# Kernel optimization log

Measured on AMD Instinct MI355X. Metric: run time of the kernel, lower is better.

The kernel has to match this reference:

```python
import jax, jax.numpy as jnp
import numpy as np

B, N, C, H = 4, 2048, 384, 8
HD = C // H  # 48; divisible by 6 so RoPE3D splits into three even-sized chunks
ROPE_BASE = 100.0  # RoPE3D(100)


def _rope1d(x, p):
    # x: [B,H,N,d], p: [B,N] integer positions
    d = x.shape[-1]
    inv = 1.0 / (ROPE_BASE ** (jnp.arange(0, d, 2, dtype=jnp.float32) / d))  # [d/2]
    ang = p[:, None, :, None].astype(jnp.float32) * inv                      # [B,1,N,d/2]
    ang = jnp.concatenate([ang, ang], axis=-1)                               # [B,1,N,d]
    cos, sin = jnp.cos(ang), jnp.sin(ang)
    x1, x2 = jnp.split(x, 2, axis=-1)
    return x * cos + jnp.concatenate([-x2, x1], axis=-1) * sin


def _rope3d(x, pos):
    # x: [B,H,N,D], pos: [B,N,3]; rotate each D/3 chunk by one spatial axis
    parts = jnp.split(x, 3, axis=-1)
    return jnp.concatenate([_rope1d(parts[i], pos[..., i]) for i in range(3)], axis=-1)


def setup_inputs() -> dict:
    key = jax.random.key(0)
    ks = jax.random.split(key, 9)
    T = B * N
    s = 1.0 / np.sqrt(C).astype(np.float32)
    offs = jnp.arange(1, B + 1, dtype=jnp.int32) * N  # equal-length segments
    return {
        "query": jax.random.normal(ks[0], (T, C), jnp.float32),
        "key": jax.random.normal(ks[1], (T, C), jnp.float32),
        "value": jax.random.normal(ks[2], (T, C), jnp.float32),
        "Wq": jax.random.normal(ks[3], (C, C), jnp.float32) * s,
        "bq": jnp.zeros((C,), jnp.float32),
        "Wk": jax.random.normal(ks[4], (C, C), jnp.float32) * s,
        "bk": jnp.zeros((C,), jnp.float32),
        "Wv": jax.random.normal(ks[5], (C, C), jnp.float32) * s,
        "bv": jnp.zeros((C,), jnp.float32),
        "Wo": jax.random.normal(ks[6], (C, C), jnp.float32) * s,
        "bo": jnp.zeros((C,), jnp.float32),
        "qpos": jax.random.randint(ks[7], (T, 3), 0, 100),
        "kpos": jax.random.randint(ks[8], (T, 3), 0, 100),
        "src_point_offset": offs,
        "tgt_point_offset": offs,
    }


def reference(query, key, value, Wq, bq, Wk, bk, Wv, bv, Wo, bo,
              qpos, kpos, src_point_offset, tgt_point_offset):
    # Equal-length segments (offsets = [N,2N,...]) => the per-item python loop
    # in forward_pcd_to_pcd is exactly one batched attention over [B,N,C].
    qb = query.reshape(B, N, C)
    kb = key.reshape(B, N, C)
    vb = value.reshape(B, N, C)
    q = (qb @ Wq.T + bq).reshape(B, N, H, HD).transpose(0, 2, 1, 3)  # [B,H,N,HD]
    k = (kb @ Wk.T + bk).reshape(B, N, H, HD).transpose(0, 2, 1, 3)
    v = (vb @ Wv.T + bv).reshape(B, N, H, HD).transpose(0, 2, 1, 3)
    q = _rope3d(q, qpos.reshape(B, N, 3))
    k = _rope3d(k, kpos.reshape(B, N, 3))
    scale = 1.0 / np.sqrt(HD).astype(np.float32)
    attn = jax.nn.softmax(jnp.einsum("bhqd,bhkd->bhqk", q, k) * scale, axis=-1)
    x = jnp.einsum("bhqk,bhkd->bhqd", attn, v)  # [B,H,N,HD]
    x = x.transpose(0, 2, 1, 3).reshape(B * N, C)
    return x @ Wo.T + bo
```

## Files before the change

kernel.cpp:

```cpp
#include <hip/hip_runtime.h>
#include <hip/hip_bf16.h>
#include <math.h>


typedef __attribute__((ext_vector_type(8))) short bf16x8;
typedef __attribute__((ext_vector_type(4))) float f32x4;
typedef __attribute__((ext_vector_type(4))) short s16x4;

__device__ inline short f2bf(float f) {
    unsigned u = __float_as_uint(f);
    u += 0x7fffu + ((u >> 16) & 1u);
    return (short)(u >> 16);
}
__device__ inline unsigned pk_bf16(float a, float b) {
    __hip_bfloat162 h = __float22bfloat162_rn(make_float2(a, b));
    return *(reinterpret_cast<unsigned*>(&h));
}
__device__ inline unsigned pk2(float lo, float hi) {
    return (__float_as_uint(lo) >> 16) | (__float_as_uint(hi) & 0xffff0000u);
}
__device__ inline float bflo(unsigned u) { return __uint_as_float(u << 16); }
__device__ inline float bfhi(unsigned u) { return __uint_as_float(u & 0xffff0000u); }
__device__ inline float exp2f_fast(float x) {
#if __has_builtin(__builtin_amdgcn_exp2f)
    return __builtin_amdgcn_exp2f(x);
#else
    return exp2f(x);
#endif
}
__device__ inline float ffract(float x) {
    float r;
    asm("v_fract_f32 %0, %1" : "=v"(r) : "v"(x));
    return r;
}
__device__ inline float fsin(float x) {
    float r;
    asm("v_sin_f32 %0, %1\n\ts_nop 1" : "=v"(r) : "v"(x));
    return r;
}
__device__ inline float fcos(float x) {
    float r;
    asm("v_cos_f32 %0, %1\n\ts_nop 1" : "=v"(r) : "v"(x));
    return r;
}
__device__ inline int div48(int c) { return (c * 683) >> 15; }

__global__ __launch_bounds__(256)
void cvt_w(const float* __restrict__ w0, const float* __restrict__ w1,
           const float* __restrict__ w2, const float* __restrict__ w3,
           short* __restrict__ Wh, short* __restrict__ Wl)
{
    const float* s = blockIdx.y == 0 ? w0 : blockIdx.y == 1 ? w1
                   : blockIdx.y == 2 ? w2 : w3;
    const size_t base = (size_t)blockIdx.y * 147456;
    const size_t i = (size_t)(blockIdx.x * 256 + threadIdx.x) * 4;
    const float4 x = *(const float4*)(s + i);
    const unsigned h01 = pk2(x.x, x.y);
    const unsigned h23 = pk2(x.z, x.w);
    uint2 hv; hv.x = h01; hv.y = h23;
    uint2 lv;
    lv.x = pk2(x.x - bflo(h01), x.y - bfhi(h01));
    lv.y = pk2(x.z - bflo(h23), x.w - bfhi(h23));
    *(uint2*)(Wh + base + i) = hv;
    *(uint2*)(Wl + base + i) = lv;
}

__global__ __launch_bounds__(256)
void gemm_qkv(const float* __restrict__ q_in, const float* __restrict__ k_in,
              const float* __restrict__ v_in,
              const short* __restrict__ Whp, const short* __restrict__ Wlp,
              const float* __restrict__ bq, const float* __restrict__ bk,
              const float* __restrict__ bv,
              const int* __restrict__ qpos, const int* __restrict__ kpos,
              short* __restrict__ qp0, short* __restrict__ qtb,
              short* __restrict__ kp0, short* __restrict__ ktb,
              short* __restrict__ vp)
{
    __shared__ short Wls[2][128 * 40];

    const int z = blockIdx.z;
    const float* A = z == 0 ? q_in : z == 1 ? k_in : v_in;
    const short* Wh = Whp + (size_t)z * 147456;
    const short* Wl = Wlp + (size_t)z * 147456;
    const float* bias = z == 0 ? bq : z == 1 ? bk : bv;

    const int tid = threadIdx.x;
    const int wv = tid >> 6, lane = tid & 63;
    const int l15 = lane & 15, quad = lane >> 4;
    const int mb = blockIdx.x * 64 + (wv & 1) * 32;
    const int nbl = (wv >> 1) * 64;
    const int n0 = blockIdx.y * 128;

    const int srow = tid >> 1;
    const int sh = (tid & 1) * 16;
    const short* wg_h = Wh + (size_t)(n0 + srow) * 384 + sh;
    const short* wg_l = Wl + (size_t)(n0 + srow) * 384 + sh;
    short* ds_h = &Wls[0][srow * 40 + sh];
    short* ds_l = &Wls[1][srow * 40 + sh];

    f32x4 acc[2][4] = {};
    const float* a0 = A + (size_t)(mb + l15) * 384 + quad * 8;

    for (int ks = 0; ks < 12; ++ks) {
        const int o = ks * 32;
        __syncthreads();
        *(bf16x8*)(ds_h)     = *(const bf16x8*)(wg_h + o);
        *(bf16x8*)(ds_h + 8) = *(const bf16x8*)(wg_h + o + 8);
        *(bf16x8*)(ds_l)     = *(const bf16x8*)(wg_l + o);
        *(bf16x8*)(ds_l + 8) = *(const bf16x8*)(wg_l + o + 8);
        bf16x8 ah[2], al[2];
        #pragma unroll
        for (int mt = 0; mt < 2; ++mt) {
            const float4 x0 = *(const float4*)(a0 + o + mt * 16 * 384);
            const float4 x1 = *(const float4*)(a0 + o + mt * 16 * 384 + 4);
            union { bf16x8 v; unsigned u[4]; } ch, cl;
            ch.u[0] = pk2(x0.x, x0.y);
            ch.u[1] = pk2(x0.z, x0.w);
            ch.u[2] = pk2(x1.x, x1.y);
            ch.u[3] = pk2(x1.z, x1.w);
            cl.u[0] = pk2(x0.x - bflo(ch.u[0]), x0.y - bfhi(ch.u[0]));
            cl.u[1] = pk2(x0.z - bflo(ch.u[1]), x0.w - bfhi(ch.u[1]));
            cl.u[2] = pk2(x1.x - bflo(ch.u[2]), x1.y - bfhi(ch.u[2]));
            cl.u[3] = pk2(x1.z - bflo(ch.u[3]), x1.w - bfhi(ch.u[3]));
            ah[mt] = ch.v;
            al[mt] = cl.v;
        }
        __syncthreads();

        #pragma unroll
        for (int nt = 0; nt < 4; ++nt) {
            const int wr = (nbl + nt * 16 + l15) * 40 + quad * 8;
            const bf16x8 wh = *(const bf16x8*)&Wls[0][wr];
            const bf16x8 wl = *(const bf16x8*)&Wls[1][wr];
            #pragma unroll
            for (int mt = 0; mt < 2; ++mt) {
                acc[mt][nt] = __builtin_amdgcn_mfma_f32_16x16x32_bf16(
                    ah[mt], wh, acc[mt][nt], 0, 0, 0);
                acc[mt][nt] = __builtin_amdgcn_mfma_f32_16x16x32_bf16(
                    al[mt], wh, acc[mt][nt], 0, 0, 0);
                acc[mt][nt] = __builtin_amdgcn_mfma_f32_16x16x32_bf16(
                    ah[mt], wl, acc[mt][nt], 0, 0, 0);
            }
        }
    }

    if (z < 2) {
        const int* pos = z ? kpos : qpos;
        const float oscale = z ? 1.0f : 0.2082339551542919f;
        const float invf = exp2f_fast(-(float)(l15 & 7) * 0.8304820237218405f)
                         * 0.15915494309189535f;
        const bool lo_half = (l15 < 8);
        #pragma unroll
        for (int nt = 0; nt < 4; ++nt) {
            const int c = n0 + nbl + nt * 16 + l15;
            const int h = div48(c);
            const int r0 = c - h * 48;
            const int axis = r0 >> 4;
            const float bb = bias[c];
            #pragma unroll
            for (int mt = 0; mt < 2; ++mt) {
                float a[4], pr[4];
                #pragma unroll
                for (int r = 0; r < 4; ++r) a[r] = acc[mt][nt][r] + bb;
                #pragma unroll
                for (int r = 0; r < 4; ++r) pr[r] = __shfl_xor(a[r], 8);
                #pragma unroll
                for (int r = 0; r < 4; ++r) {
                    const int t = mb + mt * 16 + quad * 4 + r;
                    const float pp = (float)pos[t * 3 + axis];
                    const float fr = ffract(pp * invf);
                    const float sn = fsin(fr), cn = fcos(fr);
                    const float o2 = lo_half ? (a[r] * cn - pr[r] * sn)
                                             : (a[r] * cn + pr[r] * sn);
                    const short val = f2bf(o2 * oscale);
                    const int b = t >> 11, n = t & 2047;
                    const int bh_ = b * 8 + h;
                    if (r0 < 32) {
                        short* pbuf = z ? kp0 : qp0;
                        pbuf[(((size_t)bh_ * 128 + (n >> 4)) * 64
                              + (r0 >> 3) * 16 + (n & 15)) * 8 + (r0 & 7)] = val;
                    } else if (z == 0) {
                        const int dd = r0 - 32;
                        qtb[(((size_t)bh_ * 128 + (n >> 4)) * 32
                             + (dd >> 3) * 16 + (n & 15)) * 8 + (dd & 7)] = val;
                    } else {
                        const int dd = r0 - 32;
                        ktb[(((size_t)bh_ * 64 + (n >> 5)) * 64
                             + ((n >> 4) & 1) * 32 + (dd >> 3) * 16 + (n & 15)) * 8
                            + (dd & 7)] = val;
                    }
                }
            }
        }
    } else {
        #pragma unroll
        for (int nt = 0; nt < 4; ++nt) {
            const int c = n0 + nbl + nt * 16 + l15;
            const int h = div48(c);
            const int r0 = c - h * 48;
            const float bb = bias[c];
            #pragma unroll
            for (int mt = 0; mt < 2; ++mt) {
                const int t0 = mb + mt * 16 + quad * 4;
                const int b = t0 >> 11, n = t0 & 2047;
                const int bh_ = b * 8 + h;
                s16x4 pk;
                #pragma unroll
                for (int r = 0; r < 4; ++r)
                    ((short*)&pk)[r] = f2bf(acc[mt][nt][r] + bb);
                const size_t off =
                    ((((size_t)bh_ * 16 + (n >> 7)) * 3 + (r0 >> 4)) * 4
                     + ((n >> 5) & 3)) * 512
                    + (((n >> 3) & 3) * 16 + (r0 & 15)) * 8 + (n & 7);
                *(s16x4*)(vp + off) = pk;
            }
        }
    }
}

__global__ __launch_bounds__(256)
void gemm_out(const short* __restrict__ xh, const short* __restrict__ xl,
              const short* __restrict__ Whp, const short* __restrict__ Wlp,
              const float* __restrict__ bo, float* __restrict__ out)
{
    __shared__ short Wls[2][128 * 40];

    const short* Wh = Whp + (size_t)3 * 147456;
    const short* Wl = Wlp + (size_t)3 * 147456;

    const int tid = threadIdx.x;
    const int wv = tid >> 6, lane = tid & 63;
    const int l15 = lane & 15, quad = lane >> 4;
    const int mb = blockIdx.x * 64 + (wv & 1) * 32;
    const int nbl = (wv >> 1) * 64;
    const int n0 = blockIdx.y * 128;

    const int srow = tid >> 1;
    const int sh = (tid & 1) * 16;
    const short* wg_h = Wh + (size_t)(n0 + srow) * 384 + sh;
    const short* wg_l = Wl + (size_t)(n0 + srow) * 384 + sh;
    short* ds_h = &Wls[0][srow * 40 + sh];
    short* ds_l = &Wls[1][srow * 40 + sh];

    f32x4 acc[2][4] = {};
    const short* a0 = xh + (size_t)(mb + l15) * 384 + quad * 8;
    const short* a1 = xl + (size_t)(mb + l15) * 384 + quad * 8;

    for (int ks = 0; ks < 12; ++ks) {
        const int o = ks * 32;
        __syncthreads();
        *(bf16x8*)(ds_h)     = *(const bf16x8*)(wg_h + o);
        *(bf16x8*)(ds_h + 8) = *(const bf16x8*)(wg_h + o + 8);
        *(bf16x8*)(ds_l)     = *(const bf16x8*)(wg_l + o);
        *(bf16x8*)(ds_l + 8) = *(const bf16x8*)(wg_l + o + 8);
        bf16x8 ah[2], al[2];
        #pragma unroll
        for (int mt = 0; mt < 2; ++mt) {
            ah[mt] = *(const bf16x8*)(a0 + o + mt * 16 * 384);
            al[mt] = *(const bf16x8*)(a1 + o + mt * 16 * 384);
        }
        __syncthreads();

        #pragma unroll
        for (int nt = 0; nt < 4; ++nt) {
            const int wr = (nbl + nt * 16 + l15) * 40 + quad * 8;
            const bf16x8 wh = *(const bf16x8*)&Wls[0][wr];
            const bf16x8 wl = *(const bf16x8*)&Wls[1][wr];
            #pragma unroll
            for (int mt = 0; mt < 2; ++mt) {
                acc[mt][nt] = __builtin_amdgcn_mfma_f32_16x16x32_bf16(
                    ah[mt], wh, acc[mt][nt], 0, 0, 0);
                acc[mt][nt] = __builtin_amdgcn_mfma_f32_16x16x32_bf16(
                    al[mt], wh, acc[mt][nt], 0, 0, 0);
                acc[mt][nt] = __builtin_amdgcn_mfma_f32_16x16x32_bf16(
                    ah[mt], wl, acc[mt][nt], 0, 0, 0);
            }
        }
    }

    #pragma unroll
    for (int nt = 0; nt < 4; ++nt) {
        const int c = n0 + nbl + nt * 16 + l15;
        const float bb = bo[c];
        #pragma unroll
        for (int mt = 0; mt < 2; ++mt)
            #pragma unroll
            for (int r = 0; r < 4; ++r)
                out[(size_t)(mb + mt * 16 + quad * 4 + r) * 384 + c] =
                    acc[mt][nt][r] + bb;
    }
}

__global__ __launch_bounds__(256)
void attn_mfma(const short* __restrict__ Qp0, const short* __restrict__ Qt,
               const short* __restrict__ Kp0, const short* __restrict__ Kt,
               const short* __restrict__ Vp,
               short* __restrict__ x2h, short* __restrict__ x2l)
{
    __shared__ short Ps[4][16][136];
    const int tid = threadIdx.x;
    const int wave = tid >> 6;
    const int lane = tid & 63;
    const int l15 = lane & 15;
    const int quad = lane >> 4;
    const int L = blockIdx.x;
    const int bh = (L & 7) + ((L >> 8) << 3);
    const int q0 = ((L >> 3) & 31) << 6;

    const int qt16 = (q0 >> 4) + wave;
    const bf16x8 qb0 = *(const bf16x8*)
        (Qp0 + (((size_t)bh * 128 + qt16) * 64 + lane) * 8);
    const bf16x8 qtl = *(const bf16x8*)
        (Qt + (((size_t)bh * 128 + qt16) * 32 + (lane & 31)) * 8);
    const bf16x8 z8 = {0, 0, 0, 0, 0, 0, 0, 0};
    const bf16x8 qb1lo = (quad < 2) ? qtl : z8;
    const bf16x8 qb1hi = (quad < 2) ? z8 : qtl;

    f32x4 of[3];
    #pragma unroll
    for (int t = 0; t < 3; ++t) of[t] = (f32x4){0.f, 0.f, 0.f, 0.f};
    f32x4 lsv = (f32x4){0.f, 0.f, 0.f, 0.f};

    for (int kt = 0; kt < 16; ++kt) {
        const short* kb = Kp0 + (((size_t)bh * 128 + kt * 8) * 64 + lane) * 8;
        const short* kq = Kt + (((size_t)bh * 64 + kt * 4) * 64 + lane) * 8;
        f32x4 sf[8];
        #pragma unroll
        for (int p = 0; p < 4; ++p) {
            const bf16x8 ka0 = *(const bf16x8*)(kb + (2 * p) * 512);
            const bf16x8 ka1 = *(const bf16x8*)(kb + (2 * p + 1) * 512);
            const bf16x8 kts = *(const bf16x8*)(kq + p * 512);
            f32x4 z0 = (f32x4){0.f, 0.f, 0.f, 0.f};
            z0 = __builtin_amdgcn_mfma_f32_16x16x32_bf16(ka0, qb0, z0, 0, 0, 0);
            sf[2 * p] = __builtin_amdgcn_mfma_f32_16x16x32_bf16(kts, qb1lo, z0, 0, 0, 0);
            f32x4 z1 = (f32x4){0.f, 0.f, 0.f, 0.f};
            z1 = __builtin_amdgcn_mfma_f32_16x16x32_bf16(ka1, qb0, z1, 0, 0, 0);
            sf[2 * p + 1] = __builtin_amdgcn_mfma_f32_16x16x32_bf16(kts, qb1hi, z1, 0, 0, 0);
        }

        #pragma unroll
        for (int t = 0; t < 8; ++t) {
            const float p0 = exp2f_fast(sf[t][0]);
            const float p1 = exp2f_fast(sf[t][1]);
            const float p2 = exp2f_fast(sf[t][2]);
            const float p3 = exp2f_fast(sf[t][3]);
            lsv[0] += p0; lsv[1] += p1; lsv[2] += p2; lsv[3] += p3;
            uint2 w;
            w.x = pk_bf16(p0, p1);
            w.y = pk_bf16(p2, p3);
            *(uint2*)&Ps[wave][l15][t * 16 + quad * 4] = w;
        }

        const short* vb = Vp + (((size_t)bh * 16 + kt) * 12 * 64 + lane) * 8;
        bf16x8 pb[4];
        #pragma unroll
        for (int s = 0; s < 4; ++s)
            pb[s] = *(const bf16x8*)&Ps[wave][l15][s * 32 + quad * 8];
        #pragma unroll
        for (int t = 0; t < 3; ++t) {
            #pragma unroll
            for (int s = 0; s < 4; ++s) {
                const bf16x8 va = *(const bf16x8*)(vb + (t * 4 + s) * 512);
                of[t] = __builtin_amdgcn_mfma_f32_16x16x32_bf16(va, pb[s], of[t], 0, 0, 0);
            }
        }
    }

    float ls = (lsv[0] + lsv[1]) + (lsv[2] + lsv[3]);
    ls += __shfl_xor(ls, 16);
    ls += __shfl_xor(ls, 32);
    const float invl = 1.0f / ls;
    const int b = bh >> 3, h = bh & 7;
    const size_t off = (size_t)(b * 2048 + q0 + wave * 16 + l15) * 384
                     + h * 48 + quad * 4;
    #pragma unroll
    for (int t = 0; t < 3; ++t) {
        const float o0 = of[t][0] * invl;
        const float o1 = of[t][1] * invl;
        const float o2 = of[t][2] * invl;
        const float o3 = of[t][3] * invl;
        const unsigned h01 = pk_bf16(o0, o1);
        const unsigned h23 = pk_bf16(o2, o3);
        uint2 hv; hv.x = h01; hv.y = h23;
        uint2 lv;
        lv.x = pk2(o0 - bflo(h01), o1 - bfhi(h01));
        lv.y = pk2(o2 - bflo(h23), o3 - bfhi(h23));
        *(uint2*)(x2h + off + t * 16) = hv;
        *(uint2*)(x2l + off + t * 16) = lv;
    }
}

extern "C" void kernel_launch(void* const* d_in, const int* in_sizes, int n_in,
                              void* d_out, int out_size, void* d_ws, size_t ws_size,
                              hipStream_t stream)
{
    const float* query = (const float*)d_in[0];
    const float* key_  = (const float*)d_in[1];
    const float* value = (const float*)d_in[2];
    const float* Wq = (const float*)d_in[3];
    const float* bq = (const float*)d_in[4];
    const float* Wk = (const float*)d_in[5];
    const float* bk = (const float*)d_in[6];
    const float* Wv = (const float*)d_in[7];
    const float* bv = (const float*)d_in[8];
    const float* Wo = (const float*)d_in[9];
    const float* bo = (const float*)d_in[10];
    const int* qpos = (const int*)d_in[11];
    const int* kpos = (const int*)d_in[12];

    const size_t QP0_S = (size_t)32 * 128 * 64 * 8;
    const size_t QT_S  = (size_t)32 * 128 * 32 * 8;
    const size_t KP0_S = QP0_S;
    const size_t KT_S  = (size_t)32 * 64 * 64 * 8;
    const size_t VP_S  = (size_t)32 * 16 * 12 * 64 * 8;
    const size_t X2_S  = (size_t)8192 * 384;
    const size_t W_S   = (size_t)4 * 384 * 384;

    short* w = (short*)d_ws;
    short* qp0 = w;  w += QP0_S;
    short* qtb = w;  w += QT_S;
    short* kp0 = w;  w += KP0_S;
    short* ktb = w;  w += KT_S;
    short* vp  = w;  w += VP_S;
    short* x2h = w;  w += X2_S;
    short* x2l = w;  w += X2_S;
    short* Wh  = w;  w += W_S;
    short* Wl  = w;

    const dim3 blk(256);
    cvt_w<<<dim3(144, 4), blk, 0, stream>>>(Wq, Wk, Wv, Wo, Wh, Wl);
    gemm_qkv<<<dim3(128, 3, 3), blk, 0, stream>>>(
        query, key_, value, Wh, Wl, bq, bk, bv, qpos, kpos,
        qp0, qtb, kp0, ktb, vp);
    attn_mfma<<<dim3(1024), blk, 0, stream>>>(qp0, qtb, kp0, ktb, vp, x2h, x2l);
    gemm_out<<<dim3(128, 3), blk, 0, stream>>>(x2h, x2l, Wh, Wl, bo,
                                               (float*)d_out);
}
```

Baseline: 235.0 us.

## Split attention key range across wave pairs and reduce partials in LDS

Each attention block now covers 32 queries instead of 64. Its four waves form two pairs, and each pair processes half of the key tiles for the same 16-query tile. The upper waves write their partial output accumulators and row sums to shared memory, which reuses the P buffer through a union. The lower waves add these partials and normalise before storing. The grid doubles to 2048 blocks to add parallelism and shorten each wave's serial key loop, at the cost of two barriers, an LDS reduction, and half the waves idling during the epilogue.

```diff
diff --git a/kernel.cpp b/kernel.cpp
--- a/kernel.cpp
+++ b/kernel.cpp
@@ -297,17 +297,23 @@
                const short* __restrict__ Vp,
                short* __restrict__ x2h, short* __restrict__ x2l)
 {
-    __shared__ short Ps[4][16][136];
+    __shared__ __align__(16) union {
+        short ps[4][16][136];
+        struct { float oc[2][3][64][4]; float lc[2][64]; } c;
+    } sm;
+
     const int tid = threadIdx.x;
     const int wave = tid >> 6;
     const int lane = tid & 63;
     const int l15 = lane & 15;
     const int quad = lane >> 4;
     const int L = blockIdx.x;
-    const int bh = (L & 7) + ((L >> 8) << 3);
-    const int q0 = ((L >> 3) & 31) << 6;
-
-    const int qt16 = (q0 >> 4) + wave;
+    const int bh = (L & 7) + ((L >> 9) << 3);
+    const int q0 = ((L >> 3) & 63) << 5;
+    const int qt = wave & 1;
+    const int kh = wave >> 1;
+
+    const int qt16 = (q0 >> 4) + qt;
     const bf16x8 qb0 = *(const bf16x8*)
         (Qp0 + (((size_t)bh * 128 + qt16) * 64 + lane) * 8);
     const bf16x8 qtl = *(const bf16x8*)
@@ -321,7 +327,8 @@
     for (int t = 0; t < 3; ++t) of[t] = (f32x4){0.f, 0.f, 0.f, 0.f};
     f32x4 lsv = (f32x4){0.f, 0.f, 0.f, 0.f};
 
-    for (int kt = 0; kt < 16; ++kt) {
+    const int kt0 = kh * 8;
+    for (int kt = kt0; kt < kt0 + 8; ++kt) {
         const short* kb = Kp0 + (((size_t)bh * 128 + kt * 8) * 64 + lane) * 8;
         const short* kq = Kt + (((size_t)bh * 64 + kt * 4) * 64 + lane) * 8;
         f32x4 sf[8];
@@ -348,14 +355,14 @@
             uint2 w;
             w.x = pk_bf16(p0, p1);
             w.y = pk_bf16(p2, p3);
-            *(uint2*)&Ps[wave][l15][t * 16 + quad * 4] = w;
+            *(uint2*)&sm.ps[wave][l15][t * 16 + quad * 4] = w;
         }
 
         const short* vb = Vp + (((size_t)bh * 16 + kt) * 12 * 64 + lane) * 8;
         bf16x8 pb[4];
         #pragma unroll
         for (int s = 0; s < 4; ++s)
-            pb[s] = *(const bf16x8*)&Ps[wave][l15][s * 32 + quad * 8];
+            pb[s] = *(const bf16x8*)&sm.ps[wave][l15][s * 32 + quad * 8];
         #pragma unroll
         for (int t = 0; t < 3; ++t) {
             #pragma unroll
@@ -369,24 +376,40 @@
     float ls = (lsv[0] + lsv[1]) + (lsv[2] + lsv[3]);
     ls += __shfl_xor(ls, 16);
     ls += __shfl_xor(ls, 32);
-    const float invl = 1.0f / ls;
-    const int b = bh >> 3, h = bh & 7;
-    const size_t off = (size_t)(b * 2048 + q0 + wave * 16 + l15) * 384
-                     + h * 48 + quad * 4;
-    #pragma unroll
-    for (int t = 0; t < 3; ++t) {
-        const float o0 = of[t][0] * invl;
-        const float o1 = of[t][1] * invl;
-        const float o2 = of[t][2] * invl;
-        const float o3 = of[t][3] * invl;
-        const unsigned h01 = pk_bf16(o0, o1);
-        const unsigned h23 = pk_bf16(o2, o3);
-        uint2 hv; hv.x = h01; hv.y = h23;
-        uint2 lv;
-        lv.x = pk2(o0 - bflo(h01), o1 - bfhi(h01));
-        lv.y = pk2(o2 - bflo(h23), o3 - bfhi(h23));
-        *(uint2*)(x2h + off + t * 16) = hv;
-        *(uint2*)(x2l + off + t * 16) = lv;
+
+    __syncthreads();
+    if (wave >= 2) {
+        #pragma unroll
+        for (int t = 0; t < 3; ++t)
+            *(f32x4*)&sm.c.oc[qt][t][lane][0] = of[t];
+        sm.c.lc[qt][lane] = ls;
+    }
+    __syncthreads();
+    if (wave < 2) {
+        #pragma unroll
+        for (int t = 0; t < 3; ++t)
+            of[t] += *(const f32x4*)&sm.c.oc[qt][t][lane][0];
+        ls += sm.c.lc[qt][lane];
+
+        const float invl = 1.0f / ls;
+        const int b = bh >> 3, h = bh & 7;
+        const size_t off = (size_t)(b * 2048 + q0 + qt * 16 + l15) * 384
+                         + h * 48 + quad * 4;
+        #pragma unroll
+        for (int t = 0; t < 3; ++t) {
+            const float o0 = of[t][0] * invl;
+            const float o1 = of[t][1] * invl;
+            const float o2 = of[t][2] * invl;
+            const float o3 = of[t][3] * invl;
+            const unsigned h01 = pk_bf16(o0, o1);
+            const unsigned h23 = pk_bf16(o2, o3);
+            uint2 hv; hv.x = h01; hv.y = h23;
+            uint2 lv;
+            lv.x = pk2(o0 - bflo(h01), o1 - bfhi(h01));
+            lv.y = pk2(o2 - bflo(h23), o3 - bfhi(h23));
+            *(uint2*)(x2h + off + t * 16) = hv;
+            *(uint2*)(x2l + off + t * 16) = lv;
+        }
     }
 }
 
@@ -432,7 +455,7 @@
     gemm_qkv<<<dim3(128, 3, 3), blk, 0, stream>>>(
         query, key_, value, Wh, Wl, bq, bk, bv, qpos, kpos,
         qp0, qtb, kp0, ktb, vp);
-    attn_mfma<<<dim3(1024), blk, 0, stream>>>(qp0, qtb, kp0, ktb, vp, x2h, x2l);
+    attn_mfma<<<dim3(2048), blk, 0, stream>>>(qp0, qtb, kp0, ktb, vp, x2h, x2l);
     gemm_out<<<dim3(128, 3), blk, 0, stream>>>(x2h, x2l, Wh, Wl, bo,
                                                (float*)d_out);
 }
```

After: 234.9 us. No clear change (-0.0%).

## Split attention key range across wave pairs, each wave handling two query tiles

Applied to the files above, without the earlier changes.

Each wave now processes two 16-row query tiles over half of the key range instead of one query tile over the full range. Every K and V fragment loaded from global memory is reused for two query tiles, halving per-wave global load traffic. The two key-half partial outputs and row sums are combined through shared memory (unioned with the P staging buffer) after a block barrier. The price is more register pressure (launch bounds now request 3 blocks per CU), two extra __syncthreads, and only half the waves doing the final normalization and store.

```diff
diff --git a/kernel.cpp b/kernel.cpp
--- a/kernel.cpp
+++ b/kernel.cpp
@@ -291,13 +291,17 @@
     }
 }
 
-__global__ __launch_bounds__(256)
+__global__ __launch_bounds__(256, 3)
 void attn_mfma(const short* __restrict__ Qp0, const short* __restrict__ Qt,
                const short* __restrict__ Kp0, const short* __restrict__ Kt,
                const short* __restrict__ Vp,
                short* __restrict__ x2h, short* __restrict__ x2l)
 {
-    __shared__ short Ps[4][16][136];
+    __shared__ __align__(16) union {
+        short ps[4][2][16][136];
+        struct { float oc[2][2][3][64][4]; float lc[2][2][64]; } c;
+    } sm;
+
     const int tid = threadIdx.x;
     const int wave = tid >> 6;
     const int lane = tid & 63;
@@ -306,87 +310,164 @@
     const int L = blockIdx.x;
     const int bh = (L & 7) + ((L >> 8) << 3);
     const int q0 = ((L >> 3) & 31) << 6;
-
-    const int qt16 = (q0 >> 4) + wave;
-    const bf16x8 qb0 = *(const bf16x8*)
+    const int qp = wave & 1;
+    const int kh = wave >> 1;
+
+    const int qt16 = (q0 >> 4) + qp * 2;
+    const bf16x8 qb0A = *(const bf16x8*)
         (Qp0 + (((size_t)bh * 128 + qt16) * 64 + lane) * 8);
-    const bf16x8 qtl = *(const bf16x8*)
+    const bf16x8 qb0B = *(const bf16x8*)
+        (Qp0 + (((size_t)bh * 128 + qt16 + 1) * 64 + lane) * 8);
+    const bf16x8 qtlA = *(const bf16x8*)
         (Qt + (((size_t)bh * 128 + qt16) * 32 + (lane & 31)) * 8);
+    const bf16x8 qtlB = *(const bf16x8*)
+        (Qt + (((size_t)bh * 128 + qt16 + 1) * 32 + (lane & 31)) * 8);
     const bf16x8 z8 = {0, 0, 0, 0, 0, 0, 0, 0};
-    const bf16x8 qb1lo = (quad < 2) ? qtl : z8;
-    const bf16x8 qb1hi = (quad < 2) ? z8 : qtl;
-
-    f32x4 of[3];
+    const bf16x8 qb1loA = (quad < 2) ? qtlA : z8;
+    const bf16x8 qb1hiA = (quad < 2) ? z8 : qtlA;
+    const bf16x8 qb1loB = (quad < 2) ? qtlB : z8;
+    const bf16x8 qb1hiB = (quad < 2) ? z8 : qtlB;
+
+    f32x4 ofA[3], ofB[3];
     #pragma unroll
-    for (int t = 0; t < 3; ++t) of[t] = (f32x4){0.f, 0.f, 0.f, 0.f};
-    f32x4 lsv = (f32x4){0.f, 0.f, 0.f, 0.f};
-
-    for (int kt = 0; kt < 16; ++kt) {
+    for (int t = 0; t < 3; ++t) {
+        ofA[t] = (f32x4){0.f, 0.f, 0.f, 0.f};
+        ofB[t] = (f32x4){0.f, 0.f, 0.f, 0.f};
+    }
+    f32x4 lsvA = (f32x4){0.f, 0.f, 0.f, 0.f};
+    f32x4 lsvB = (f32x4){0.f, 0.f, 0.f, 0.f};
+
+    const int kt0 = kh * 8;
+    for (int kt = kt0; kt < kt0 + 8; ++kt) {
         const short* kb = Kp0 + (((size_t)bh * 128 + kt * 8) * 64 + lane) * 8;
         const short* kq = Kt + (((size_t)bh * 64 + kt * 4) * 64 + lane) * 8;
-        f32x4 sf[8];
         #pragma unroll
         for (int p = 0; p < 4; ++p) {
             const bf16x8 ka0 = *(const bf16x8*)(kb + (2 * p) * 512);
             const bf16x8 ka1 = *(const bf16x8*)(kb + (2 * p + 1) * 512);
             const bf16x8 kts = *(const bf16x8*)(kq + p * 512);
-            f32x4 z0 = (f32x4){0.f, 0.f, 0.f, 0.f};
-            z0 = __builtin_amdgcn_mfma_f32_16x16x32_bf16(ka0, qb0, z0, 0, 0, 0);
-            sf[2 * p] = __builtin_amdgcn_mfma_f32_16x16x32_bf16(kts, qb1lo, z0, 0, 0, 0);
-            f32x4 z1 = (f32x4){0.f, 0.f, 0.f, 0.f};
-            z1 = __builtin_amdgcn_mfma_f32_16x16x32_bf16(ka1, qb0, z1, 0, 0, 0);
-            sf[2 * p + 1] = __builtin_amdgcn_mfma_f32_16x16x32_bf16(kts, qb1hi, z1, 0, 0, 0);
-        }
-
-        #pragma unroll
-        for (int t = 0; t < 8; ++t) {
-            const float p0 = exp2f_fast(sf[t][0]);
-            const float p1 = exp2f_fast(sf[t][1]);
-            const float p2 = exp2f_fast(sf[t][2]);
-            const float p3 = exp2f_fast(sf[t][3]);
-            lsv[0] += p0; lsv[1] += p1; lsv[2] += p2; lsv[3] += p3;
-            uint2 w;
-            w.x = pk_bf16(p0, p1);
-            w.y = pk_bf16(p2, p3);
-            *(uint2*)&Ps[wave][l15][t * 16 + quad * 4] = w;
+            f32x4 s0, s1, s2, s3;
+            s0 = (f32x4){0.f, 0.f, 0.f, 0.f};
+            s0 = __builtin_amdgcn_mfma_f32_16x16x32_bf16(ka0, qb0A, s0, 0, 0, 0);
+            s0 = __builtin_amdgcn_mfma_f32_16x16x32_bf16(kts, qb1loA, s0, 0, 0, 0);
+            s1 = (f32x4){0.f, 0.f, 0.f, 0.f};
+            s1 = __builtin_amdgcn_mfma_f32_16x16x32_bf16(ka1, qb0A, s1, 0, 0, 0);
+            s1 = __builtin_amdgcn_mfma_f32_16x16x32_bf16(kts, qb1hiA, s1, 0, 0, 0);
+            s2 = (f32x4){0.f, 0.f, 0.f, 0.f};
+            s2 = __builtin_amdgcn_mfma_f32_16x16x32_bf16(ka0, qb0B, s2, 0, 0, 0);
+            s2 = __builtin_amdgcn_mfma_f32_16x16x32_bf16(kts, qb1loB, s2, 0, 0, 0);
+            s3 = (f32x4){0.f, 0.f, 0.f, 0.f};
+            s3 = __builtin_amdgcn_mfma_f32_16x16x32_bf16(ka1, qb0B, s3, 0, 0, 0);
+            s3 = __builtin_amdgcn_mfma_f32_16x16x32_bf16(kts, qb1hiB, s3, 0, 0, 0);
+
+            {
+                const float p0 = exp2f_fast(s0[0]), p1 = exp2f_fast(s0[1]);
+                const float p2 = exp2f_fast(s0[2]), p3 = exp2f_fast(s0[3]);
+                lsvA[0] += p0; lsvA[1] += p1; lsvA[2] += p2; lsvA[3] += p3;
+                uint2 w; w.x = pk_bf16(p0, p1); w.y = pk_bf16(p2, p3);
+                *(uint2*)&sm.ps[wave][0][l15][(2 * p) * 16 + quad * 4] = w;
+            }
+            {
+                const float p0 = exp2f_fast(s1[0]), p1 = exp2f_fast(s1[1]);
+                const float p2 = exp2f_fast(s1[2]), p3 = exp2f_fast(s1[3]);
+                lsvA[0] += p0; lsvA[1] += p1; lsvA[2] += p2; lsvA[3] += p3;
+                uint2 w; w.x = pk_bf16(p0, p1); w.y = pk_bf16(p2, p3);
+                *(uint2*)&sm.ps[wave][0][l15][(2 * p + 1) * 16 + quad * 4] = w;
+            }
+            {
+                const float p0 = exp2f_fast(s2[0]), p1 = exp2f_fast(s2[1]);
+                const float p2 = exp2f_fast(s2[2]), p3 = exp2f_fast(s2[3]);
+                lsvB[0] += p0; lsvB[1] += p1; lsvB[2] += p2; lsvB[3] += p3;
+                uint2 w; w.x = pk_bf16(p0, p1); w.y = pk_bf16(p2, p3);
+                *(uint2*)&sm.ps[wave][1][l15][(2 * p) * 16 + quad * 4] = w;
+            }
+            {
+                const float p0 = exp2f_fast(s3[0]), p1 = exp2f_fast(s3[1]);
+                const float p2 = exp2f_fast(s3[2]), p3 = exp2f_fast(s3[3]);
+                lsvB[0] += p0; lsvB[1] += p1; lsvB[2] += p2; lsvB[3] += p3;
+                uint2 w; w.x = pk_bf16(p0, p1); w.y = pk_bf16(p2, p3);
+                *(uint2*)&sm.ps[wave][1][l15][(2 * p + 1) * 16 + quad * 4] = w;
+            }
         }
 
         const short* vb = Vp + (((size_t)bh * 16 + kt) * 12 * 64 + lane) * 8;
-        bf16x8 pb[4];
-        #pragma unroll
-        for (int s = 0; s < 4; ++s)
-            pb[s] = *(const bf16x8*)&Ps[wave][l15][s * 32 + quad * 8];
+        #pragma unroll
+        for (int s = 0; s < 4; ++s) {
+            const bf16x8 pbA = *(const bf16x8*)&sm.ps[wave][0][l15][s * 32 + quad * 8];
+            const bf16x8 pbB = *(const bf16x8*)&sm.ps[wave][1][l15][s * 32 + quad * 8];
+            #pragma unroll
+            for (int t = 0; t < 3; ++t) {
+                const bf16x8 va = *(const bf16x8*)(vb + (t * 4 + s) * 512);
+                ofA[t] = __builtin_amdgcn_mfma_f32_16x16x32_bf16(va, pbA, ofA[t], 0, 0, 0);
+                ofB[t] = __builtin_amdgcn_mfma_f32_16x16x32_bf16(va, pbB, ofB[t], 0, 0, 0);
+            }
+        }
+    }
+
+    float lsA = (lsvA[0] + lsvA[1]) + (lsvA[2] + lsvA[3]);
+    lsA += __shfl_xor(lsA, 16);
+    lsA += __shfl_xor(lsA, 32);
+    float lsB = (lsvB[0] + lsvB[1]) + (lsvB[2] + lsvB[3]);
+    lsB += __shfl_xor(lsB, 16);
+    lsB += __shfl_xor(lsB, 32);
+
+    __syncthreads();
+    if (kh == 1) {
         #pragma unroll
         for (int t = 0; t < 3; ++t) {
-            #pragma unroll
-            for (int s = 0; s < 4; ++s) {
-                const bf16x8 va = *(const bf16x8*)(vb + (t * 4 + s) * 512);
-                of[t] = __builtin_amdgcn_mfma_f32_16x16x32_bf16(va, pb[s], of[t], 0, 0, 0);
-            }
-        }
-    }
-
-    float ls = (lsv[0] + lsv[1]) + (lsv[2] + lsv[3]);
-    ls += __shfl_xor(ls, 16);
-    ls += __shfl_xor(ls, 32);
-    const float invl = 1.0f / ls;
-    const int b = bh >> 3, h = bh & 7;
-    const size_t off = (size_t)(b * 2048 + q0 + wave * 16 + l15) * 384
-                     + h * 48 + quad * 4;
-    #pragma unroll
-    for (int t = 0; t < 3; ++t) {
-        const float o0 = of[t][0] * invl;
-        const float o1 = of[t][1] * invl;
-        const float o2 = of[t][2] * invl;
-        const float o3 = of[t][3] * invl;
-        const unsigned h01 = pk_bf16(o0, o1);
-        const unsigned h23 = pk_bf16(o2, o3);
-        uint2 hv; hv.x = h01; hv.y = h23;
-        uint2 lv;
-        lv.x = pk2(o0 - bflo(h01), o1 - bfhi(h01));
-        lv.y = pk2(o2 - bflo(h23), o3 - bfhi(h23));
-        *(uint2*)(x2h + off + t * 16) = hv;
-        *(uint2*)(x2l + off + t * 16) = lv;
+            *(f32x4*)&sm.c.oc[qp][0][t][lane][0] = ofA[t];
+            *(f32x4*)&sm.c.oc[qp][1][t][lane][0] = ofB[t];
+        }
+        sm.c.lc[qp][0][lane] = lsA;
+        sm.c.lc[qp][1][lane] = lsB;
+    }
+    __syncthreads();
+    if (kh == 0) {
+        #pragma unroll
+        for (int t = 0; t < 3; ++t) {
+            ofA[t] += *(const f32x4*)&sm.c.oc[qp][0][t][lane][0];
+            ofB[t] += *(const f32x4*)&sm.c.oc[qp][1][t][lane][0];
+        }
+        lsA += sm.c.lc[qp][0][lane];
+        lsB += sm.c.lc[qp][1][lane];
+
+        const int b = bh >> 3, h = bh & 7;
+        const float invlA = 1.0f / lsA;
+        const float invlB = 1.0f / lsB;
+        const size_t offA = (size_t)(b * 2048 + q0 + (qp * 2) * 16 + l15) * 384
+                          + h * 48 + quad * 4;
+        const size_t offB = offA + 16 * 384;
+        #pragma unroll
+        for (int t = 0; t < 3; ++t) {
+            {
+                const float o0 = ofA[t][0] * invlA;
+                const float o1 = ofA[t][1] * invlA;
+                const float o2 = ofA[t][2] * invlA;
+                const float o3 = ofA[t][3] * invlA;
+                const unsigned h01 = pk_bf16(o0, o1);
+                const unsigned h23 = pk_bf16(o2, o3);
+                uint2 hv; hv.x = h01; hv.y = h23;
+                uint2 lv;
+                lv.x = pk2(o0 - bflo(h01), o1 - bfhi(h01));
+                lv.y = pk2(o2 - bflo(h23), o3 - bfhi(h23));
+                *(uint2*)(x2h + offA + t * 16) = hv;
+                *(uint2*)(x2l + offA + t * 16) = lv;
+            }
+            {
+                const float o0 = ofB[t][0] * invlB;
+                const float o1 = ofB[t][1] * invlB;
+                const float o2 = ofB[t][2] * invlB;
+                const float o3 = ofB[t][3] * invlB;
+                const unsigned h01 = pk_bf16(o0, o1);
+                const unsigned h23 = pk_bf16(o2, o3);
+                uint2 hv; hv.x = h01; hv.y = h23;
+                uint2 lv;
+                lv.x = pk2(o0 - bflo(h01), o1 - bfhi(h01));
+                lv.y = pk2(o2 - bflo(h23), o3 - bfhi(h23));
+                *(uint2*)(x2h + offB + t * 16) = hv;
+                *(uint2*)(x2l + offB + t * 16) = lv;
+            }
+        }
     }
 }
 
```

New measurement: 249.1 us. +6.0%, slower.
